# Kernel optimization log

Hardware: AMD Instinct MI355X
Metric: run time of the kernel (lower is better)

## Reference

```python
import jax, jax.numpy as jnp
import numpy as np
from jax import lax

NPOINT = 2048
RADIUS = 0.1
NSAMPLE = 32


def setup_inputs() -> dict:
    key = jax.random.key(0)
    ks = jax.random.split(key, 6)
    B, N, C = 8, 16384, 16
    xyz = jax.random.uniform(ks[0], (B, N, 3), dtype=jnp.float32)
    features = jax.random.normal(ks[1], (B, N, C), dtype=jnp.float32)
    W1 = jax.random.normal(ks[2], (C, 32), dtype=jnp.float32) * 0.1
    b1 = jnp.zeros((32,), jnp.float32)
    W2 = jax.random.normal(ks[3], (32, 32), dtype=jnp.float32) * 0.1
    b2 = jnp.zeros((32,), jnp.float32)
    W3 = jax.random.normal(ks[4], (32, 64), dtype=jnp.float32) * 0.1
    b3 = jnp.zeros((64,), jnp.float32)
    return {"xyz": xyz, "features": features,
            "W1": W1, "b1": b1, "W2": W2, "b2": b2, "W3": W3, "b3": b3}


def farthest_point_sample(xyz, npoint):
    # Sequential FPS: keep running min-distance to selected set, argmax each step.
    B, N, _ = xyz.shape

    def step(carry, _):
        min_d, far = carry  # min_d: [B,N], far: [B]
        centroid = jnp.take_along_axis(xyz, far[:, None, None], axis=1)  # [B,1,3]
        d = jnp.sum((xyz - centroid) ** 2, axis=-1)                      # [B,N]
        min_d = jnp.minimum(min_d, d)
        nxt = jnp.argmax(min_d, axis=1).astype(jnp.int32)
        return (min_d, nxt), far

    init = (jnp.full((B, N), 1e10, xyz.dtype), jnp.zeros((B,), jnp.int32))
    _, idx = lax.scan(step, init, None, length=npoint)  # idx: [npoint, B]
    return idx.T  # [B, npoint]


def ball_query(radius, nsample, xyz, new_xyz):
    # Squared pairwise distances [B, S, N]
    d2 = (jnp.sum(new_xyz ** 2, -1)[:, :, None]
          + jnp.sum(xyz ** 2, -1)[:, None, :]
          - 2.0 * jnp.einsum('bsd,bnd->bsn', new_xyz, xyz))
    N = xyz.shape[1]
    # Take the first `nsample` in-ball indices (by point order), pad with first found.
    scores = jnp.where(d2 <= radius * radius,
                       jnp.arange(N, dtype=jnp.int32), jnp.int32(N))
    vals = -lax.top_k(-scores, nsample)[0]  # smallest nsample scores, ascending
    first = vals[..., :1]                   # center itself is always in-ball
    return jnp.where(vals == N, first, vals)  # [B, S, nsample] int32


def reference(xyz, features, W1, b1, W2, b2, W3, b3):
    fps_idx = farthest_point_sample(xyz, NPOINT)                      # [B,S]
    new_xyz = jnp.take_along_axis(xyz, fps_idx[..., None], axis=1)    # [B,S,3]
    idx = ball_query(RADIUS, NSAMPLE, xyz, new_xyz)                   # [B,S,K]
    grouped = jax.vmap(lambda f, i: f[i])(features, idx)              # [B,S,K,C]
    h = jax.nn.relu(grouped @ W1 + b1)
    h = jax.nn.relu(h @ W2 + b2)
    h = h @ W3 + b3                                                   # [B,S,K,64]
    new_features = jnp.max(h, axis=2)                                 # [B,S,64]
    return new_xyz, new_features
```

## Files before the change

### kernel.cpp

```cpp
#include <hip/hip_runtime.h>

#define B 8
#define N 16384
#define S 2048
#define NS 32
#define CIN 16
#define NCELL 512

typedef float f32x2 __attribute__((ext_vector_type(2)));
typedef int   i32x2 __attribute__((ext_vector_type(2)));

template<int CTRL>
__device__ __forceinline__ float dpp_fmax(float x) {
    int t = __builtin_amdgcn_update_dpp(0, __float_as_int(x), CTRL, 0xF, 0xF, true);
    return fmaxf(x, __int_as_float(t));
}
template<int CTRL>
__device__ __forceinline__ unsigned dpp_umax(unsigned x) {
    unsigned t = (unsigned)__builtin_amdgcn_update_dpp(0, (int)x, CTRL, 0xF, 0xF, true);
    return x > t ? x : t;
}
__device__ __forceinline__ float wave_fmax(float x) {
    x = dpp_fmax<0xB1>(x);
    x = dpp_fmax<0x4E>(x);
    x = dpp_fmax<0x114>(x);
    x = dpp_fmax<0x118>(x);
    x = dpp_fmax<0x142>(x);
    x = dpp_fmax<0x143>(x);
    return __int_as_float(__builtin_amdgcn_readlane(__float_as_int(x), 63));
}
__device__ __forceinline__ unsigned wave_umax(unsigned x) {
    x = dpp_umax<0xB1>(x);
    x = dpp_umax<0x4E>(x);
    x = dpp_umax<0x114>(x);
    x = dpp_umax<0x118>(x);
    x = dpp_umax<0x142>(x);
    x = dpp_umax<0x143>(x);
    return (unsigned)__builtin_amdgcn_readlane((int)x, 63);
}

__device__ __forceinline__ int expand3(int v) {
    return (v & 1) | ((v & 2) << 2) | ((v & 4) << 4);
}

__global__ __launch_bounds__(1024) void bucket_kernel(const float* __restrict__ xyz,
                                                      float* __restrict__ Xp,
                                                      float* __restrict__ Yp,
                                                      float* __restrict__ Zp,
                                                      int* __restrict__ Ip) {
    const int b = blockIdx.x;
    const int t = threadIdx.x;
    const float* xb = xyz + (size_t)b * N * 3;

    __shared__ int hist[NCELL], pA[NCELL], pB[NCELL], run[NCELL];
    if (t < NCELL) { hist[t] = 0; run[t] = 0; }
    __syncthreads();

    int cell[16];
    float xs[16], ys[16], zs[16];
#pragma unroll
    for (int k = 0; k < 16; ++k) {
        const int n = t + (k << 10);
        const float x = xb[3 * n + 0];
        const float y = xb[3 * n + 1];
        const float z = xb[3 * n + 2];
        int cx = min(7, max(0, (int)(x * 8.0f)));
        int cy = min(7, max(0, (int)(y * 8.0f)));
        int cz = min(7, max(0, (int)(z * 8.0f)));
        const int c = expand3(cx) | (expand3(cy) << 1) | (expand3(cz) << 2);
        cell[k] = c; xs[k] = x; ys[k] = y; zs[k] = z;
        atomicAdd(&hist[c], 1);
    }
    __syncthreads();

    int* cur = pA; int* nxt = pB;
    if (t < NCELL) cur[t] = hist[t];
    __syncthreads();
    for (int off = 1; off < NCELL; off <<= 1) {
        if (t < NCELL) nxt[t] = cur[t] + ((t >= off) ? cur[t - off] : 0);
        __syncthreads();
        int* tmp = cur; cur = nxt; nxt = tmp;
    }
    if (t < NCELL) nxt[t] = cur[t] - hist[t];
    __syncthreads();
    const int* base = nxt;

#pragma unroll
    for (int k = 0; k < 16; ++k) {
        const int c = cell[k];
        const int pos = base[c] + atomicAdd(&run[c], 1);
        const size_t o = (size_t)b * N + pos;
        Xp[o] = xs[k]; Yp[o] = ys[k]; Zp[o] = zs[k];
        Ip[o] = t + (k << 10);
    }
}

__global__ __launch_bounds__(1024, 1) void fps_prune_kernel(const float* __restrict__ xyz,
                                                            const float* __restrict__ Xp,
                                                            const float* __restrict__ Yp,
                                                            const float* __restrict__ Zp,
                                                            const int* __restrict__ Ip,
                                                            float* __restrict__ new_xyz) {
#pragma clang fp contract(off)
    const int b = blockIdx.x;
    const int t = threadIdx.x;
    const float* xb = xyz + (size_t)b * N * 3;
    const size_t base = (size_t)b * N + ((size_t)t << 4);

    f32x2 px[8], py[8], pz[8], md[8];
    i32x2 ip[8];
    {
        const f32x2* X2 = (const f32x2*)(Xp + base);
        const f32x2* Y2 = (const f32x2*)(Yp + base);
        const f32x2* Z2 = (const f32x2*)(Zp + base);
        const i32x2* I2 = (const i32x2*)(Ip + base);
#pragma unroll
        for (int j = 0; j < 8; ++j) {
            px[j] = X2[j]; py[j] = Y2[j]; pz[j] = Z2[j]; ip[j] = I2[j];
            md[j] = (f32x2){1e10f, 1e10f};
        }
    }

    float lox = px[0].x, hix = px[0].x, loy = py[0].x, hiy = py[0].x,
          loz = pz[0].x, hiz = pz[0].x;
#pragma unroll
    for (int j = 0; j < 8; ++j) {
        lox = fminf(lox, fminf(px[j].x, px[j].y)); hix = fmaxf(hix, fmaxf(px[j].x, px[j].y));
        loy = fminf(loy, fminf(py[j].x, py[j].y)); hiy = fmaxf(hiy, fmaxf(py[j].x, py[j].y));
        loz = fminf(loz, fminf(pz[j].x, pz[j].y)); hiz = fmaxf(hiz, fmaxf(pz[j].x, pz[j].y));
    }

    __shared__ unsigned long long slot3[3];
    if (t == 0) { slot3[0] = 0ull; slot3[1] = 0ull; slot3[2] = 0ull; }
    __syncthreads();

    int p = 0;
    float ub = 1e10f;
    int cand = ip[0].x;
    unsigned long long wkey = 0ull;
    float cx = xb[0], cy = xb[1], cz = xb[2];

    for (int it = 0; it < S; ++it) {
        if (t == 0) {
            float* o = new_xyz + ((size_t)b * S + it) * 3;
            o[0] = cx; o[1] = cy; o[2] = cz;
        }
        const float ddx = fmaxf(0.0f, fmaxf(lox - cx, cx - hix));
        const float ddy = fmaxf(0.0f, fmaxf(loy - cy, cy - hiy));
        const float ddz = fmaxf(0.0f, fmaxf(loz - cz, cz - hiz));
        const float lb = (ddx * ddx + ddy * ddy) + ddz * ddz;
        const bool upd = !(lb * 0.99998f > ub);

        if (__any(upd)) {
            if (upd) {
                asm volatile("" : "+v"(px[0]), "+v"(px[1]), "+v"(px[2]), "+v"(px[3]),
                                  "+v"(px[4]), "+v"(px[5]), "+v"(px[6]), "+v"(px[7]));
                asm volatile("" : "+v"(py[0]), "+v"(py[1]), "+v"(py[2]), "+v"(py[3]),
                                  "+v"(py[4]), "+v"(py[5]), "+v"(py[6]), "+v"(py[7]));
                asm volatile("" : "+v"(pz[0]), "+v"(pz[1]), "+v"(pz[2]), "+v"(pz[3]),
                                  "+v"(pz[4]), "+v"(pz[5]), "+v"(pz[6]), "+v"(pz[7]));
                asm volatile("" : "+v"(ip[0]), "+v"(ip[1]), "+v"(ip[2]), "+v"(ip[3]),
                                  "+v"(ip[4]), "+v"(ip[5]), "+v"(ip[6]), "+v"(ip[7]));
                const f32x2 c2x = {cx, cx}, c2y = {cy, cy}, c2z = {cz, cz};
                float nu = 0.0f;
#pragma unroll
                for (int j = 0; j < 8; ++j) {
                    const f32x2 dx = px[j] - c2x;
                    const f32x2 dy = py[j] - c2y;
                    const f32x2 dz = pz[j] - c2z;
                    const f32x2 xx = dx * dx;
                    const f32x2 yy = dy * dy;
                    const f32x2 zz = dz * dz;
                    const f32x2 ss = xx + yy;
                    const f32x2 dd = ss + zz;
                    f32x2 m;
                    m.x = fminf(md[j].x, dd.x);
                    m.y = fminf(md[j].y, dd.y);
                    md[j] = m;
                    nu = fmaxf(nu, fmaxf(m.x, m.y));
                }
                int c = 0x7fffffff;
#pragma unroll
                for (int j = 0; j < 8; ++j) {
                    if (md[j].x == nu) c = min(c, ip[j].x);
                    if (md[j].y == nu) c = min(c, ip[j].y);
                }
                ub = nu; cand = c;
            }
            const float wmax = wave_fmax(ub);
            unsigned cn = (ub == wmax) ? ~(unsigned)cand : 0u;
            cn = wave_umax(cn);
            wkey = ((unsigned long long)__float_as_uint(wmax) << 32)
                 | (unsigned long long)cn;
        }
        if ((t & 63) == 0) atomicMax(&slot3[p], wkey);
        int pn = p + 1; if (pn == 3) pn = 0;
        if (t == 0) slot3[pn] = 0ull;
        __syncthreads();
        const unsigned long long r = slot3[p];
        const int far = (int)(~(unsigned)r);
        cx = xb[3 * far + 0];
        cy = xb[3 * far + 1];
        cz = xb[3 * far + 2];
        p = pn;
    }
}

__global__ __launch_bounds__(1024) void fps_kernel(const float* __restrict__ xyz,
                                                   float* __restrict__ new_xyz) {
#pragma clang fp contract(off)
    const int b = blockIdx.x;
    const int t = threadIdx.x;
    const float* xb = xyz + (size_t)b * N * 3;

    float px[16], py[16], pz[16], md[16];
#pragma unroll
    for (int k = 0; k < 16; ++k) {
        const int n = t + (k << 10);
        px[k] = xb[3 * n + 0];
        py[k] = xb[3 * n + 1];
        pz[k] = xb[3 * n + 2];
        md[k] = 1e10f;
    }
    __shared__ float rv[2][16];
    __shared__ int slot[2];
    if (t == 0) { slot[0] = 0x7fffffff; slot[1] = 0x7fffffff; }
    __syncthreads();
    int far = 0, p = 0;
    const int lane = t & 63, w = t >> 6;
    for (int it = 0; it < S; ++it) {
        const float cx = xb[3 * far + 0], cy = xb[3 * far + 1], cz = xb[3 * far + 2];
        if (t == 0) {
            float* o = new_xyz + ((size_t)b * S + it) * 3;
            o[0] = cx; o[1] = cy; o[2] = cz;
        }
        float bestv = -1.0f;
#pragma unroll
        for (int k = 0; k < 16; ++k) {
            const float dx = __fsub_rn(px[k], cx);
            const float dy = __fsub_rn(py[k], cy);
            const float dz = __fsub_rn(pz[k], cz);
            const float d  = __fadd_rn(__fadd_rn(__fmul_rn(dx, dx), __fmul_rn(dy, dy)),
                                       __fmul_rn(dz, dz));
            const float m = fminf(md[k], d);
            md[k] = m;
            bestv = fmaxf(bestv, m);
        }
        float v = bestv;
#pragma unroll
        for (int off = 32; off >= 1; off >>= 1) v = fmaxf(v, __shfl_xor(v, off));
        if (lane == 0) rv[p][w] = v;
        __syncthreads();
        float u = rv[p][lane & 15];
#pragma unroll
        for (int off = 8; off >= 1; off >>= 1) u = fmaxf(u, __shfl_xor(u, off));
        if (t == 0) slot[p ^ 1] = 0x7fffffff;
        if (bestv == u) {
            int cnd2 = 0x7fffffff;
#pragma unroll
            for (int k = 0; k < 16; ++k)
                if (md[k] == u) cnd2 = min(cnd2, t + (k << 10));
            atomicMin(&slot[p], cnd2);
        }
        __syncthreads();
        far = slot[p];
        p ^= 1;
    }
}

__global__ __launch_bounds__(64) void ball_mlp_kernel(
    const float* __restrict__ xyz,
    const float* __restrict__ feat,
    const float* __restrict__ W1, const float* __restrict__ b1,
    const float* __restrict__ W2, const float* __restrict__ b2,
    const float* __restrict__ W3, const float* __restrict__ b3,
    const float* __restrict__ new_xyz,
    float* __restrict__ out_feat) {
#pragma clang fp contract(off)
    const int q = blockIdx.x;
    const int b = q >> 11;
    const int lane = threadIdx.x;
    const float* xb = xyz + (size_t)b * N * 3;

    const double qx = (double)new_xyz[3 * q + 0];
    const double qy = (double)new_xyz[3 * q + 1];
    const double qz = (double)new_xyz[3 * q + 2];
    const double s2 = qx * qx + qy * qy + qz * qz;
    const double R2 = 0.1 * 0.1;

    __shared__ int idxbuf[NS];
    int found = 0;
    for (int bs = 0; bs < N; bs += 64) {
        const int n = bs + lane;
        const double x = (double)xb[3 * n + 0];
        const double y = (double)xb[3 * n + 1];
        const double z = (double)xb[3 * n + 2];
        const double n2 = x * x + y * y + z * z;
        const double dt = qx * x + qy * y + qz * z;
        const double d2 = (s2 + n2) - 2.0 * dt;
        const bool ok = (d2 <= R2);
        const unsigned long long msk = __ballot(ok);
        if (ok) {
            const int pos = found + (int)__popcll(msk & ((1ull << lane) - 1ull));
            if (pos < NS) idxbuf[pos] = n;
        }
        found += (int)__popcll(msk);
        if (found >= NS) break;
    }
    __syncthreads();
    if (lane == 0) {
        const int cnt = found < NS ? found : NS;
        const int first = (cnt > 0) ? idxbuf[0] : (N - 1);
        for (int j2 = cnt; j2 < NS; ++j2) idxbuf[j2] = first;
    }
    __syncthreads();

    const int j = lane & 31;
    const int h = lane >> 5;
    const int nid = idxbuf[j];
    const float* fp = feat + ((size_t)b * N + nid) * CIN;
    float fv[CIN];
#pragma unroll
    for (int k = 0; k < CIN; ++k) fv[k] = fp[k];

    float h1[32];
#pragma unroll
    for (int c = 0; c < 32; ++c) {
        float a = b1[c];
#pragma unroll
        for (int k = 0; k < CIN; ++k) a = fmaf(fv[k], W1[(k << 5) + c], a);
        h1[c] = fmaxf(a, 0.0f);
    }
    float h2[32];
#pragma unroll
    for (int c = 0; c < 32; ++c) {
        float a = b2[c];
#pragma unroll
        for (int k = 0; k < 32; ++k) a = fmaf(h1[k], W2[(k << 5) + c], a);
        h2[c] = fmaxf(a, 0.0f);
    }
    const int cbase = h << 5;
    float mx[32];
#pragma unroll
    for (int c = 0; c < 32; ++c) {
        float a = b3[cbase + c];
#pragma unroll
        for (int k = 0; k < 32; ++k) a = fmaf(h2[k], W3[(k << 6) + cbase + c], a);
        mx[c] = a;
    }
#pragma unroll
    for (int off = 1; off <= 16; off <<= 1) {
#pragma unroll
        for (int c = 0; c < 32; ++c) mx[c] = fmaxf(mx[c], __shfl_xor(mx[c], off));
    }
    if (j == 0) {
        float* o = out_feat + (size_t)q * 64 + cbase;
#pragma unroll
        for (int c = 0; c < 32; ++c) o[c] = mx[c];
    }
}

extern "C" void kernel_launch(void* const* d_in, const int* in_sizes, int n_in,
                              void* d_out, int out_size, void* d_ws, size_t ws_size,
                              hipStream_t stream) {
    (void)in_sizes; (void)n_in; (void)out_size;
    const float* xyz  = (const float*)d_in[0];
    const float* feat = (const float*)d_in[1];
    const float* W1   = (const float*)d_in[2];
    const float* b1   = (const float*)d_in[3];
    const float* W2   = (const float*)d_in[4];
    const float* b2   = (const float*)d_in[5];
    const float* W3   = (const float*)d_in[6];
    const float* b3   = (const float*)d_in[7];

    float* out      = (float*)d_out;
    float* new_xyz  = out;
    float* new_feat = out + (size_t)B * S * 3;

    const size_t need = (size_t)4 * B * N * sizeof(float);
    if (ws_size >= need) {
        float* Xp = (float*)d_ws;
        float* Yp = Xp + (size_t)B * N;
        float* Zp = Yp + (size_t)B * N;
        int*   Ip = (int*)(Zp + (size_t)B * N);
        bucket_kernel<<<B, 1024, 0, stream>>>(xyz, Xp, Yp, Zp, Ip);
        fps_prune_kernel<<<B, 1024, 0, stream>>>(xyz, Xp, Yp, Zp, Ip, new_xyz);
    } else {
        fps_kernel<<<B, 1024, 0, stream>>>(xyz, new_xyz);
    }
    ball_mlp_kernel<<<B * S, 64, 0, stream>>>(xyz, feat, W1, b1, W2, b2, W3, b3,
                                              new_xyz, new_feat);
}
```

Baseline: 2.362 ms.

## Refine spatial grid to 16^3 cells and vectorize FPS min/max updates

Raises the Morton-ordered bucketing grid from 8^3 to 16^3 cells, so each thread's slice of points in the pruned FPS is spatially tighter. The scan is rewritten so each thread owns four cells. Tighter cell bounds let the lower-bound test skip more distance updates. The FPS inner loop now uses packed elementwise min/max, and the selected index is made wave-uniform via readfirstlane so centroid loads go through scalar memory. The finer grid costs more shared memory and scan work, and the per-iteration changes are small.

```diff
diff --git a/kernel.cpp b/kernel.cpp
--- a/kernel.cpp
+++ b/kernel.cpp
@@ -5,7 +5,7 @@
 #define S 2048
 #define NS 32
 #define CIN 16
-#define NCELL 512
+#define NCELL 4096
 
 typedef float f32x2 __attribute__((ext_vector_type(2)));
 typedef int   i32x2 __attribute__((ext_vector_type(2)));
@@ -39,8 +39,8 @@
     return (unsigned)__builtin_amdgcn_readlane((int)x, 63);
 }
 
-__device__ __forceinline__ int expand3(int v) {
-    return (v & 1) | ((v & 2) << 2) | ((v & 4) << 4);
+__device__ __forceinline__ int expand4(int v) {
+    return (v & 1) | ((v & 2) << 2) | ((v & 4) << 4) | ((v & 8) << 6);
 }
 
 __global__ __launch_bounds__(1024) void bucket_kernel(const float* __restrict__ xyz,
@@ -52,8 +52,10 @@
     const int t = threadIdx.x;
     const float* xb = xyz + (size_t)b * N * 3;
 
-    __shared__ int hist[NCELL], pA[NCELL], pB[NCELL], run[NCELL];
-    if (t < NCELL) { hist[t] = 0; run[t] = 0; }
+    __shared__ int hist[NCELL];
+    __shared__ int run[NCELL];
+    __shared__ int pA[1024], pB[1024];
+    for (int i = t; i < NCELL; i += 1024) { hist[i] = 0; run[i] = 0; }
     __syncthreads();
 
     int cell[16];
@@ -64,31 +66,38 @@
         const float x = xb[3 * n + 0];
         const float y = xb[3 * n + 1];
         const float z = xb[3 * n + 2];
-        int cx = min(7, max(0, (int)(x * 8.0f)));
-        int cy = min(7, max(0, (int)(y * 8.0f)));
-        int cz = min(7, max(0, (int)(z * 8.0f)));
-        const int c = expand3(cx) | (expand3(cy) << 1) | (expand3(cz) << 2);
+        const int cx = min(15, max(0, (int)(x * 16.0f)));
+        const int cy = min(15, max(0, (int)(y * 16.0f)));
+        const int cz = min(15, max(0, (int)(z * 16.0f)));
+        const int c = expand4(cx) | (expand4(cy) << 1) | (expand4(cz) << 2);
         cell[k] = c; xs[k] = x; ys[k] = y; zs[k] = z;
         atomicAdd(&hist[c], 1);
     }
     __syncthreads();
 
+    const int h0 = hist[4 * t + 0], h1 = hist[4 * t + 1],
+              h2 = hist[4 * t + 2], h3 = hist[4 * t + 3];
+    const int lsum = h0 + h1 + h2 + h3;
+    pA[t] = lsum;
+    __syncthreads();
     int* cur = pA; int* nxt = pB;
-    if (t < NCELL) cur[t] = hist[t];
-    __syncthreads();
-    for (int off = 1; off < NCELL; off <<= 1) {
-        if (t < NCELL) nxt[t] = cur[t] + ((t >= off) ? cur[t - off] : 0);
+    for (int off = 1; off < 1024; off <<= 1) {
+        nxt[t] = cur[t] + ((t >= off) ? cur[t - off] : 0);
         __syncthreads();
         int* tmp = cur; cur = nxt; nxt = tmp;
     }
-    if (t < NCELL) nxt[t] = cur[t] - hist[t];
-    __syncthreads();
-    const int* base = nxt;
+    const int excl = cur[t] - lsum;
+    __syncthreads();
+    hist[4 * t + 0] = excl;
+    hist[4 * t + 1] = excl + h0;
+    hist[4 * t + 2] = excl + h0 + h1;
+    hist[4 * t + 3] = excl + h0 + h1 + h2;
+    __syncthreads();
 
 #pragma unroll
     for (int k = 0; k < 16; ++k) {
         const int c = cell[k];
-        const int pos = base[c] + atomicAdd(&run[c], 1);
+        const int pos = hist[c] + atomicAdd(&run[c], 1);
         const size_t o = (size_t)b * N + pos;
         Xp[o] = xs[k]; Yp[o] = ys[k]; Zp[o] = zs[k];
         Ip[o] = t + (k << 10);
@@ -162,23 +171,18 @@
                 asm volatile("" : "+v"(ip[0]), "+v"(ip[1]), "+v"(ip[2]), "+v"(ip[3]),
                                   "+v"(ip[4]), "+v"(ip[5]), "+v"(ip[6]), "+v"(ip[7]));
                 const f32x2 c2x = {cx, cx}, c2y = {cy, cy}, c2z = {cz, cz};
-                float nu = 0.0f;
+                f32x2 nu2 = {0.0f, 0.0f};
 #pragma unroll
                 for (int j = 0; j < 8; ++j) {
                     const f32x2 dx = px[j] - c2x;
                     const f32x2 dy = py[j] - c2y;
                     const f32x2 dz = pz[j] - c2z;
-                    const f32x2 xx = dx * dx;
-                    const f32x2 yy = dy * dy;
-                    const f32x2 zz = dz * dz;
-                    const f32x2 ss = xx + yy;
-                    const f32x2 dd = ss + zz;
-                    f32x2 m;
-                    m.x = fminf(md[j].x, dd.x);
-                    m.y = fminf(md[j].y, dd.y);
+                    const f32x2 dd = (dx * dx + dy * dy) + dz * dz;
+                    const f32x2 m = __builtin_elementwise_min(md[j], dd);
                     md[j] = m;
-                    nu = fmaxf(nu, fmaxf(m.x, m.y));
+                    nu2 = __builtin_elementwise_max(nu2, m);
                 }
+                const float nu = fmaxf(nu2.x, nu2.y);
                 int c = 0x7fffffff;
 #pragma unroll
                 for (int j = 0; j < 8; ++j) {
@@ -198,10 +202,10 @@
         if (t == 0) slot3[pn] = 0ull;
         __syncthreads();
         const unsigned long long r = slot3[p];
-        const int far = (int)(~(unsigned)r);
-        cx = xb[3 * far + 0];
-        cy = xb[3 * far + 1];
-        cz = xb[3 * far + 2];
+        const int fu = __builtin_amdgcn_readfirstlane((int)(~(unsigned)r));
+        cx = xb[3 * fu + 0];
+        cy = xb[3 * fu + 1];
+        cz = xb[3 * fu + 2];
         p = pn;
     }
 }
```

After: 2.359 ms. No clear change (-0.1%).
